# Performance work log

Hardware: AMD Instinct MI355X
Metric: run time of the kernel (lower is better)

Reference implementation:

```python
import jax, jax.numpy as jnp
import numpy as np

BATCH, INPUTDIM, OUTDIM, GRIDSIZE = 4096, 256, 256, 64


def setup_inputs() -> dict:
    key = jax.random.key(0)
    k1, k2 = jax.random.split(key)
    x = jax.random.normal(k1, (BATCH, INPUTDIM), dtype=jnp.float32)
    # xavier_uniform over (2, outdim, inputdim, gridsize): fan_in = inputdim*gridsize, fan_out = outdim*gridsize
    fan_in = INPUTDIM * GRIDSIZE
    fan_out = OUTDIM * GRIDSIZE
    limit = float(np.sqrt(6.0 / (fan_in + fan_out)))
    fouriercoeffs = jax.random.uniform(
        k2, (2, OUTDIM, INPUTDIM, GRIDSIZE), dtype=jnp.float32,
        minval=-limit, maxval=limit)
    bias = jnp.zeros((1, OUTDIM), dtype=jnp.float32)
    return {"x": x, "fouriercoeffs": fouriercoeffs, "bias": bias}


def reference(x, fouriercoeffs, bias):
    # x: [B, inputdim]; fouriercoeffs: [2, outdim, inputdim, gridsize]; bias: [1, outdim]
    # gridsize_param is clamp/round'ed to an int in torch -> static = initial_gridsize here.
    G = fouriercoeffs.shape[-1]
    k = jnp.arange(1, G + 1, dtype=x.dtype)        # [G] frequencies 1..G
    xk = x[:, :, None] * k                          # [B, inputdim, G]
    c = jnp.cos(xk)                                 # [B, inputdim, G]
    s = jnp.sin(xk)                                 # [B, inputdim, G]
    # Fused contraction over (inputdim, gridsize) -- avoids the naive
    # [B, outdim, inputdim, gridsize] broadcast tensor of the torch code.
    y = (jnp.einsum('big,oig->bo', c, fouriercoeffs[0])
         + jnp.einsum('big,oig->bo', s, fouriercoeffs[1])
         + bias)                                    # [B, outdim]
    return y
```

## Files before the change

kernel.cpp:

```cpp
#include <hip/hip_runtime.h>
#include <hip/hip_bf16.h>


typedef __attribute__((ext_vector_type(8))) short short8;
typedef __attribute__((ext_vector_type(4))) float f32x4;

#define SPLITK 8
#define ICHUNK (256 / SPLITK)

__device__ __forceinline__ unsigned short f2bf(float f) {
    unsigned u = __builtin_bit_cast(unsigned, f);
    u += 0x7fffu + ((u >> 16) & 1u);
    return (unsigned short)(u >> 16);
}
__device__ __forceinline__ unsigned pkbf16(float a, float b) {
    return (unsigned)f2bf(a) | ((unsigned)f2bf(b) << 16);
}

__device__ __forceinline__ void async_load16(const void* g, void* l) {
    __builtin_amdgcn_global_load_lds(
        (const __attribute__((address_space(1))) unsigned int*)g,
        (__attribute__((address_space(3))) unsigned int*)l,
        16, 0, 0);
}

__global__ void init_out_kernel(float* __restrict__ out, const float* __restrict__ bias) {
    int tid = blockIdx.x * 256 + threadIdx.x;
    float4 b4 = ((const float4*)bias)[tid & 63];
    ((float4*)out)[tid] = b4;
}

__global__ __launch_bounds__(256) void convert_coeffs2(
    const float* __restrict__ fc, unsigned short* __restrict__ ws2)
{
    __shared__ unsigned short lsh[256 * 72];
    const int bx = blockIdx.x;
    const int i = bx >> 1, y = bx & 1;
    const int t = threadIdx.x;

    {
        const int tt = t >> 7, op = t & 127;
        const float4* src = (const float4*)(fc +
            ((((size_t)tt * 256) + y * 128 + op) * 256 + i) * 64);
        uint4* dst = (uint4*)(lsh + t * 72);
        #pragma unroll
        for (int q2 = 0; q2 < 8; ++q2) {
            float4 a = src[q2 * 2], b = src[q2 * 2 + 1];
            uint4 v;
            v.x = pkbf16(a.x, a.y); v.y = pkbf16(a.z, a.w);
            v.z = pkbf16(b.x, b.y); v.w = pkbf16(b.z, b.w);
            dst[q2] = v;
        }
    }
    __syncthreads();

    uint4* wdst = (uint4*)ws2 + (size_t)bx * 2048;
    #pragma unroll
    for (int rep = 0; rep < 8; ++rep) {
        int gi = rep * 256 + t;
        int sog = gi >> 6, ll = gi & 63;
        int s = sog >> 3, og = sog & 7;
        int op = og * 16 + (ll & 15);
        int k = s * 32 + ((ll >> 4) * 8);
        int tt = k >> 6, g0 = k & 63;
        wdst[gi] = *(const uint4*)(lsh + (tt * 128 + op) * 72 + g0);
    }
}

template <bool USE_WS>
__global__ __launch_bounds__(256, 2) void fkan_gemm(
    const float* __restrict__ x, const float* __restrict__ fc,
    const unsigned short* __restrict__ bws, float* __restrict__ out)
{
    __shared__ uint4 Aimg[2048];
    __shared__ uint4 Bimg[2048];

    const int t  = threadIdx.x;
    const int l  = t & 63;
    const int w  = t >> 6;
    const int wr = w >> 1, wc = w & 1;
    const int rowBase = blockIdx.x * 128;
    const int by      = blockIdx.y;
    const int colBase = by * 128;
    const int iBase   = blockIdx.z * ICHUNK;
    const int fr = t & 127;
    const int tg = t >> 7;

    f32x4 acc[4][4];
    #pragma unroll
    for (int a = 0; a < 4; ++a)
        #pragma unroll
        for (int b = 0; b < 4; ++b) acc[a][b] = (f32x4)0.0f;

    const float* xrow = x + (size_t)(rowBase + fr) * 256;
    const int og = fr >> 4;
    const int lrow = fr & 15;

    auto computeA = [&](int i) {
        float xv = xrow[i];
        float s1 = __sinf(xv);
        float c1 = __cosf(xv);
        float c2 = __builtin_fmaf(2.f * c1, c1, -1.f);
        float s2 = 2.f * s1 * c1;
        float m2 = 2.f * c2;
        float cx, cy, px, py;
        if (tg == 0) { cx = c1; cy = c2; px = c1;  py = 1.f; }
        else         { cx = s1; cy = s2; px = -s1; py = 0.f; }
        #pragma unroll
        for (int oct = 0; oct < 8; ++oct) {
            unsigned pk0, pk1, pk2, pk3;
            pk0 = pkbf16(cx, cy);
            { float nx = __builtin_fmaf(m2, cx, -px), ny = __builtin_fmaf(m2, cy, -py);
              px = cx; py = cy; cx = nx; cy = ny; }
            pk1 = pkbf16(cx, cy);
            { float nx = __builtin_fmaf(m2, cx, -px), ny = __builtin_fmaf(m2, cy, -py);
              px = cx; py = cy; cx = nx; cy = ny; }
            pk2 = pkbf16(cx, cy);
            { float nx = __builtin_fmaf(m2, cx, -px), ny = __builtin_fmaf(m2, cy, -py);
              px = cx; py = cy; cx = nx; cy = ny; }
            pk3 = pkbf16(cx, cy);
            { float nx = __builtin_fmaf(m2, cx, -px), ny = __builtin_fmaf(m2, cy, -py);
              px = cx; py = cy; cx = nx; cy = ny; }
            int k = tg * 64 + oct * 8;
            int s = k >> 5;
            int q = (k >> 3) & 3;
            uint4 v; v.x = pk0; v.y = pk1; v.z = pk2; v.w = pk3;
            Aimg[(s * 8 + og) * 64 + q * 16 + lrow] = v;
        }
    };

    auto stageB_ws = [&](int i) {
        const unsigned short* base = bws + ((size_t)(i * 2 + by) * 2048) * 8;
        #pragma unroll
        for (int cc = 0; cc < 8; ++cc) {
            int c = cc * 4 + w;
            async_load16(base + (size_t)(c * 64 + l) * 8, (void*)(Bimg + c * 64));
        }
    };

    auto stageB_direct = [&](int i) {
        #pragma unroll
        for (int gg = 0; gg < 8; ++gg) {
            int gi  = gg * 256 + t;
            int sog = gi >> 6;
            int ll  = gi & 63;
            int s = sog >> 3, ogb = sog & 7;
            int o = ogb * 16 + (ll & 15);
            int k = s * 32 + (ll >> 4) * 8;
            int tt = k >> 6, g = k & 63;
            const float4* p = (const float4*)(fc +
                ((((size_t)tt * 256 + colBase + o) * 256 + i) * 64 + g));
            float4 a = p[0], b = p[1];
            uint4 v;
            v.x = pkbf16(a.x, a.y); v.y = pkbf16(a.z, a.w);
            v.z = pkbf16(b.x, b.y); v.w = pkbf16(b.z, b.w);
            Bimg[gi] = v;
        }
    };

    if (USE_WS) stageB_ws(iBase);
    computeA(iBase);
    if (!USE_WS) stageB_direct(iBase);

    #pragma unroll 1
    for (int ii = 0; ii < ICHUNK; ++ii) {
        __syncthreads();

        short8 aF[4][4], bF[4][4];
        #pragma unroll
        for (int s = 0; s < 4; ++s) {
            #pragma unroll
            for (int rf = 0; rf < 4; ++rf)
                aF[s][rf] = __builtin_bit_cast(short8, Aimg[(s * 8 + wr * 4 + rf) * 64 + l]);
            #pragma unroll
            for (int cf = 0; cf < 4; ++cf)
                bF[s][cf] = __builtin_bit_cast(short8, Bimg[(s * 8 + wc * 4 + cf) * 64 + l]);
        }

        __syncthreads();

        if (ii + 1 < ICHUNK) {
            int ni = iBase + ii + 1;
            if (USE_WS) stageB_ws(ni);
            computeA(ni);
            if (!USE_WS) stageB_direct(ni);
        }

        #pragma unroll
        for (int s = 0; s < 4; ++s)
            #pragma unroll
            for (int rf = 0; rf < 4; ++rf)
                #pragma unroll
                for (int cf = 0; cf < 4; ++cf)
                    acc[rf][cf] = __builtin_amdgcn_mfma_f32_16x16x32_bf16(
                        aF[s][rf], bF[s][cf], acc[rf][cf], 0, 0, 0);
    }

    const int lr = (l >> 4) * 4;
    const int lc = l & 15;
    const int r0 = rowBase + wr * 64 + lr;
    const int c0 = colBase + wc * 64 + lc;
    #pragma unroll
    for (int rf = 0; rf < 4; ++rf)
        #pragma unroll
        for (int cf = 0; cf < 4; ++cf)
            #pragma unroll
            for (int e = 0; e < 4; ++e)
                atomicAdd(out + (size_t)(r0 + rf * 16 + e) * 256 + (c0 + cf * 16),
                          acc[rf][cf][e]);
}

extern "C" void kernel_launch(void* const* d_in, const int* in_sizes, int n_in,
                              void* d_out, int out_size, void* d_ws, size_t ws_size,
                              hipStream_t stream) {
    const float* x    = (const float*)d_in[0];
    const float* fc   = (const float*)d_in[1];
    const float* bias = (const float*)d_in[2];
    float* out = (float*)d_out;
    unsigned short* bws = (unsigned short*)d_ws;

    hipLaunchKernelGGL(init_out_kernel, dim3(1024), dim3(256), 0, stream, out, bias);

    const size_t wsNeed = (size_t)512 * 2048 * 16;
    if (ws_size >= wsNeed) {
        hipLaunchKernelGGL(convert_coeffs2, dim3(512), dim3(256), 0, stream, fc, bws);
        hipLaunchKernelGGL((fkan_gemm<true>), dim3(32, 2, SPLITK), dim3(256), 0, stream,
                           x, fc, bws, out);
    } else {
        hipLaunchKernelGGL((fkan_gemm<false>), dim3(32, 2, SPLITK), dim3(256), 0, stream,
                           x, fc, bws, out);
    }
}
```

Before: 179.7 us.

## Generate Fourier A-fragments in registers and double-buffer B tiles

```diff
diff --git a/kernel.cpp b/kernel.cpp
--- a/kernel.cpp
+++ b/kernel.cpp
@@ -15,6 +15,39 @@
 }
 __device__ __forceinline__ unsigned pkbf16(float a, float b) {
     return (unsigned)f2bf(a) | ((unsigned)f2bf(b) << 16);
+}
+
+__device__ __forceinline__ unsigned pk_rh(float a, float b) {
+    unsigned ua = __builtin_bit_cast(unsigned, a) + 0x8000u;
+    unsigned ub = __builtin_bit_cast(unsigned, b) + 0x8000u;
+    return __builtin_amdgcn_perm(ub, ua, 0x07060302u);
+}
+
+__device__ __forceinline__ void dbl2(float c, float s, float& co, float& so) {
+    float t = c + c;
+    co = __builtin_fmaf(t, c, -1.f);
+    so = t * s;
+}
+__device__ __forceinline__ void rot2(float c, float s, float cr, float sr,
+                                     float& co, float& so) {
+    float t = s * sr;
+    co = __builtin_fmaf(c, cr, -t);
+    float u = s * cr;
+    so = __builtin_fmaf(c, sr, u);
+}
+
+__device__ __forceinline__ short8 chain8(float m1, float fm1, float f0) {
+    unsigned r[4];
+    float vp = fm1, v = f0;
+    #pragma unroll
+    for (int h = 0; h < 4; ++h) {
+        float v1 = __builtin_fmaf(m1, v, -vp);
+        r[h] = pk_rh(v, v1);
+        float v2 = __builtin_fmaf(m1, v1, -v);
+        vp = v1; v = v2;
+    }
+    uint4 u; u.x = r[0]; u.y = r[1]; u.z = r[2]; u.w = r[3];
+    return __builtin_bit_cast(short8, u);
 }
 
 __device__ __forceinline__ void async_load16(const void* g, void* l) {
@@ -37,7 +70,6 @@
     const int bx = blockIdx.x;
     const int i = bx >> 1, y = bx & 1;
     const int t = threadIdx.x;
-
     {
         const int tt = t >> 7, op = t & 127;
         const float4* src = (const float4*)(fc +
@@ -53,7 +85,6 @@
         }
     }
     __syncthreads();
-
     uint4* wdst = (uint4*)ws2 + (size_t)bx * 2048;
     #pragma unroll
     for (int rep = 0; rep < 8; ++rep) {
@@ -72,19 +103,20 @@
     const float* __restrict__ x, const float* __restrict__ fc,
     const unsigned short* __restrict__ bws, float* __restrict__ out)
 {
-    __shared__ uint4 Aimg[2048];
-    __shared__ uint4 Bimg[2048];
+    __shared__ uint4 Bimg[2][2048];
+    __shared__ float xs[ICHUNK][128];
 
     const int t  = threadIdx.x;
     const int l  = t & 63;
     const int w  = t >> 6;
     const int wr = w >> 1, wc = w & 1;
+    const int q  = l >> 4;
+    const int m  = l & 15;
     const int rowBase = blockIdx.x * 128;
     const int by      = blockIdx.y;
     const int colBase = by * 128;
     const int iBase   = blockIdx.z * ICHUNK;
-    const int fr = t & 127;
-    const int tg = t >> 7;
+    const float q8f   = (float)(q * 8);
 
     f32x4 acc[4][4];
     #pragma unroll
@@ -92,98 +124,85 @@
         #pragma unroll
         for (int b = 0; b < 4; ++b) acc[a][b] = (f32x4)0.0f;
 
-    const float* xrow = x + (size_t)(rowBase + fr) * 256;
-    const int og = fr >> 4;
-    const int lrow = fr & 15;
-
-    auto computeA = [&](int i) {
-        float xv = xrow[i];
-        float s1 = __sinf(xv);
-        float c1 = __cosf(xv);
-        float c2 = __builtin_fmaf(2.f * c1, c1, -1.f);
-        float s2 = 2.f * s1 * c1;
-        float m2 = 2.f * c2;
-        float cx, cy, px, py;
-        if (tg == 0) { cx = c1; cy = c2; px = c1;  py = 1.f; }
-        else         { cx = s1; cy = s2; px = -s1; py = 0.f; }
-        #pragma unroll
-        for (int oct = 0; oct < 8; ++oct) {
-            unsigned pk0, pk1, pk2, pk3;
-            pk0 = pkbf16(cx, cy);
-            { float nx = __builtin_fmaf(m2, cx, -px), ny = __builtin_fmaf(m2, cy, -py);
-              px = cx; py = cy; cx = nx; cy = ny; }
-            pk1 = pkbf16(cx, cy);
-            { float nx = __builtin_fmaf(m2, cx, -px), ny = __builtin_fmaf(m2, cy, -py);
-              px = cx; py = cy; cx = nx; cy = ny; }
-            pk2 = pkbf16(cx, cy);
-            { float nx = __builtin_fmaf(m2, cx, -px), ny = __builtin_fmaf(m2, cy, -py);
-              px = cx; py = cy; cx = nx; cy = ny; }
-            pk3 = pkbf16(cx, cy);
-            { float nx = __builtin_fmaf(m2, cx, -px), ny = __builtin_fmaf(m2, cy, -py);
-              px = cx; py = cy; cx = nx; cy = ny; }
-            int k = tg * 64 + oct * 8;
-            int s = k >> 5;
-            int q = (k >> 3) & 3;
-            uint4 v; v.x = pk0; v.y = pk1; v.z = pk2; v.w = pk3;
-            Aimg[(s * 8 + og) * 64 + q * 16 + lrow] = v;
+    auto stageB = [&](int p, int i) {
+        if (USE_WS) {
+            const unsigned short* base = bws + ((size_t)(i * 2 + by) * 2048) * 8;
+            #pragma unroll
+            for (int cc = 0; cc < 8; ++cc) {
+                int c = cc * 4 + w;
+                async_load16(base + (size_t)(c * 64 + l) * 8, (void*)(&Bimg[p][c * 64]));
+            }
+        } else {
+            #pragma unroll
+            for (int gg = 0; gg < 8; ++gg) {
+                int gi  = gg * 256 + t;
+                int sog = gi >> 6, ll = gi & 63;
+                int s = sog >> 3, ogb = sog & 7;
+                int o = ogb * 16 + (ll & 15);
+                int k = s * 32 + (ll >> 4) * 8;
+                int tt = k >> 6, g = k & 63;
+                const float4* p4 = (const float4*)(fc +
+                    ((((size_t)tt * 256 + colBase + o) * 256 + i) * 64 + g));
+                float4 a = p4[0], b = p4[1];
+                uint4 v;
+                v.x = pkbf16(a.x, a.y); v.y = pkbf16(a.z, a.w);
+                v.z = pkbf16(b.x, b.y); v.w = pkbf16(b.z, b.w);
+                Bimg[p][gi] = v;
+            }
         }
     };
 
-    auto stageB_ws = [&](int i) {
-        const unsigned short* base = bws + ((size_t)(i * 2 + by) * 2048) * 8;
-        #pragma unroll
-        for (int cc = 0; cc < 8; ++cc) {
-            int c = cc * 4 + w;
-            async_load16(base + (size_t)(c * 64 + l) * 8, (void*)(Bimg + c * 64));
-        }
-    };
-
-    auto stageB_direct = [&](int i) {
-        #pragma unroll
-        for (int gg = 0; gg < 8; ++gg) {
-            int gi  = gg * 256 + t;
-            int sog = gi >> 6;
-            int ll  = gi & 63;
-            int s = sog >> 3, ogb = sog & 7;
-            int o = ogb * 16 + (ll & 15);
-            int k = s * 32 + (ll >> 4) * 8;
-            int tt = k >> 6, g = k & 63;
-            const float4* p = (const float4*)(fc +
-                ((((size_t)tt * 256 + colBase + o) * 256 + i) * 64 + g));
-            float4 a = p[0], b = p[1];
-            uint4 v;
-            v.x = pkbf16(a.x, a.y); v.y = pkbf16(a.z, a.w);
-            v.z = pkbf16(b.x, b.y); v.w = pkbf16(b.z, b.w);
-            Bimg[gi] = v;
-        }
-    };
-
-    if (USE_WS) stageB_ws(iBase);
-    computeA(iBase);
-    if (!USE_WS) stageB_direct(iBase);
+    stageB(0, iBase);
+    {
+        int r = t >> 1, c0 = (t & 1) * 16;
+        const float4* px = (const float4*)(x + (size_t)(rowBase + r) * 256 + iBase + c0);
+        float4 v0 = px[0], v1 = px[1], v2 = px[2], v3 = px[3];
+        float tmp[16] = { v0.x, v0.y, v0.z, v0.w, v1.x, v1.y, v1.z, v1.w,
+                          v2.x, v2.y, v2.z, v2.w, v3.x, v3.y, v3.z, v3.w };
+        #pragma unroll
+        for (int j = 0; j < 16; ++j) xs[c0 + j][r] = tmp[j];
+    }
+    __syncthreads();
 
     #pragma unroll 1
     for (int ii = 0; ii < ICHUNK; ++ii) {
-        __syncthreads();
-
-        short8 aF[4][4], bF[4][4];
-        #pragma unroll
-        for (int s = 0; s < 4; ++s) {
-            #pragma unroll
-            for (int rf = 0; rf < 4; ++rf)
-                aF[s][rf] = __builtin_bit_cast(short8, Aimg[(s * 8 + wr * 4 + rf) * 64 + l]);
+        const int p = ii & 1;
+
+        short8 bF[4][4];
+        #pragma unroll
+        for (int s = 0; s < 4; ++s)
             #pragma unroll
             for (int cf = 0; cf < 4; ++cf)
-                bF[s][cf] = __builtin_bit_cast(short8, Bimg[(s * 8 + wc * 4 + cf) * 64 + l]);
-        }
-
-        __syncthreads();
-
-        if (ii + 1 < ICHUNK) {
-            int ni = iBase + ii + 1;
-            if (USE_WS) stageB_ws(ni);
-            computeA(ni);
-            if (!USE_WS) stageB_direct(ni);
+                bF[s][cf] = __builtin_bit_cast(short8,
+                    Bimg[p][(s * 8 + wc * 4 + cf) * 64 + l]);
+
+        if (ii + 1 < ICHUNK) stageB(p ^ 1, iBase + ii + 1);
+
+        short8 aF[4][4];
+        #pragma unroll
+        for (int rf = 0; rf < 4; ++rf) {
+            float xv = xs[ii][wr * 64 + rf * 16 + m];
+            float s1, c1;
+            __sincosf(xv, &s1, &c1);
+            const float m1 = c1 + c1;
+            float c2, s2, c4, s4, c8, s8, c16, s16, c32, s32;
+            dbl2(c1, s1, c2, s2);
+            dbl2(c2, s2, c4, s4);
+            dbl2(c4, s4, c8, s8);
+            dbl2(c8, s8, c16, s16);
+            dbl2(c16, s16, c32, s32);
+            float c24, s24;
+            rot2(c16, s16, c8, s8, c24, s24);
+            float cq = (q == 0) ? 1.f : (q == 1) ? c8 : (q == 2) ? c16 : c24;
+            float sq = (q == 0) ? 0.f : (q == 1) ? s8 : (q == 2) ? s16 : s24;
+            float cq1, sq1, cB, sB, cB1, sB1;
+            rot2(cq, sq, c1, s1, cq1, sq1);
+            rot2(cq, sq, c32, s32, cB, sB);
+            rot2(cB, sB, c1, s1, cB1, sB1);
+            aF[rf][0] = chain8(m1, cq, cq1);
+            aF[rf][1] = chain8(m1, cB, cB1);
+            aF[rf][2] = chain8(m1, sq, sq1);
+            aF[rf][3] = chain8(m1, sB, sB1);
         }
 
         #pragma unroll
@@ -193,13 +212,14 @@
                 #pragma unroll
                 for (int cf = 0; cf < 4; ++cf)
                     acc[rf][cf] = __builtin_amdgcn_mfma_f32_16x16x32_bf16(
-                        aF[s][rf], bF[s][cf], acc[rf][cf], 0, 0, 0);
+                        aF[rf][s], bF[s][cf], acc[rf][cf], 0, 0, 0);
+
+        __syncthreads();
     }
 
     const int lr = (l >> 4) * 4;
-    const int lc = l & 15;
     const int r0 = rowBase + wr * 64 + lr;
-    const int c0 = colBase + wc * 64 + lc;
+    const int c0 = colBase + wc * 64 + m;
     #pragma unroll
     for (int rf = 0; rf < 4; ++rf)
         #pragma unroll
```

Result: no change. 182.7 us (+1.7%).
